# Kernel optimization log

Hardware: AMD Instinct MI355X
Metric: run time of the kernel (lower is better)

The kernel has to match this reference:

```python
import jax, jax.numpy as jnp
import numpy as np

N_LAYERS = 8
D_MODEL = 64
D_STATE = 32
D_CONV = 4
D_INNER = 128          # expand * d_model
HEADDIM = 64
NHEADS = D_INNER // HEADDIM      # 2
CONV_DIM = D_INNER + 2 * D_STATE # 192 (x, B, C)
D_IN_PROJ = 2 * D_INNER + 2 * D_STATE + NHEADS  # 322
EPS = 1e-5


def setup_inputs() -> dict:
    key = jax.random.key(0)
    ks = jax.random.split(key, 8)
    x = jax.random.normal(ks[0], (16, 4096, D_MODEL), dtype=jnp.float32)
    Win = jax.random.normal(ks[1], (N_LAYERS, D_MODEL, D_IN_PROJ), dtype=jnp.float32) * 0.05
    conv_w = jax.random.normal(ks[2], (N_LAYERS, CONV_DIM, D_CONV), dtype=jnp.float32) * 0.2
    conv_b = jnp.zeros((N_LAYERS, CONV_DIM), dtype=jnp.float32)
    dt_bias = jax.random.uniform(ks[3], (N_LAYERS, NHEADS), minval=-4.0, maxval=-1.0)
    A_log = jnp.log(jax.random.uniform(ks[4], (N_LAYERS, NHEADS), minval=1.0, maxval=16.0))
    Dp = jnp.ones((N_LAYERS, NHEADS), dtype=jnp.float32)
    norm_w = jnp.ones((N_LAYERS, D_INNER), dtype=jnp.float32)
    Wout = jax.random.normal(ks[5], (N_LAYERS, D_INNER, D_MODEL), dtype=jnp.float32) * 0.05
    return {"x": x, "Win": Win, "conv_w": conv_w, "conv_b": conv_b,
            "dt_bias": dt_bias, "A_log": A_log, "Dp": Dp,
            "norm_w": norm_w, "Wout": Wout}


def _mamba2_layer(u, Win, conv_w, conv_b, dt_bias, A_log, Dp, norm_w, Wout):
    b, l, _ = u.shape
    zxbcdt = u @ Win                                   # (b,l,322)
    z = zxbcdt[..., :D_INNER]                          # gate (b,l,128)
    xBC = zxbcdt[..., D_INNER:D_INNER + CONV_DIM]      # (b,l,192)
    dt = jax.nn.softplus(zxbcdt[..., D_INNER + CONV_DIM:] + dt_bias)  # (b,l,H)

    # causal depthwise conv over time, then SiLU
    xc = jnp.pad(xBC.transpose(0, 2, 1), ((0, 0), (0, 0), (D_CONV - 1, 0)))
    xc = jax.lax.conv_general_dilated(
        xc, conv_w[:, None, :], (1,), 'VALID',
        feature_group_count=CONV_DIM,
        dimension_numbers=('NCH', 'OIH', 'NCH'))
    xBC = jax.nn.silu((xc + conv_b[None, :, None]).transpose(0, 2, 1))  # (b,l,192)

    xs = xBC[..., :D_INNER].reshape(b, l, NHEADS, HEADDIM)   # (b,l,h,p)
    B = xBC[..., D_INNER:D_INNER + D_STATE]                  # (b,l,n)
    C = xBC[..., D_INNER + D_STATE:]                         # (b,l,n)

    A = -jnp.exp(A_log)                                      # (h,) negative
    dA = jnp.exp(dt * A)                                     # (b,l,h)

    # sequential selective scan over time; state (b,h,p,n)
    def step(hst, inp):
        dA_t, dt_t, x_t, B_t, C_t = inp
        hst = hst * dA_t[:, :, None, None] + \
              (dt_t[:, :, None] * x_t)[..., None] * B_t[:, None, None, :]
        y_t = jnp.einsum('bhpn,bn->bhp', hst, C_t)
        return hst, y_t

    h0 = jnp.zeros((b, NHEADS, HEADDIM, D_STATE), dtype=u.dtype)
    seq = (jnp.moveaxis(dA, 1, 0), jnp.moveaxis(dt, 1, 0),
           jnp.moveaxis(xs, 1, 0), jnp.moveaxis(B, 1, 0), jnp.moveaxis(C, 1, 0))
    _, ys = jax.lax.scan(step, h0, seq)                      # (l,b,h,p)
    y = jnp.moveaxis(ys, 0, 1) + Dp[None, None, :, None] * xs  # (b,l,h,p)
    y = y.reshape(b, l, D_INNER)

    # gated RMSNorm (norm_before_gate=False): normalize after gating
    y = y * jax.nn.silu(z)
    y = y * jax.lax.rsqrt(jnp.mean(y * y, axis=-1, keepdims=True) + EPS) * norm_w
    return y @ Wout                                          # (b,l,d_model)


def reference(x, Win, conv_w, conv_b, dt_bias, A_log, Dp, norm_w, Wout):
    h = x
    for i in range(N_LAYERS - 1):
        h = _mamba2_layer(h, Win[i], conv_w[i], conv_b[i], dt_bias[i],
                          A_log[i], Dp[i], norm_w[i], Wout[i])
    h = jax.lax.stop_gradient(h)  # layers[:-1] run under torch.no_grad()
    i = N_LAYERS - 1
    return _mamba2_layer(h, Win[i], conv_w[i], conv_b[i], dt_bias[i],
                         A_log[i], Dp[i], norm_w[i], Wout[i])
```

## Files before the change

kernel.cpp:

```cpp
#include <hip/hip_runtime.h>
#include <math.h>

#define BATCH   16
#define SEQ     4096
#define DMODEL  64
#define DINNER  128
#define DSTATE  32
#define NHEADS  2
#define HEADDIM 64
#define CONVDIM 192
#define PROJ    322
#define QC      64
#define NCHUNK  (SEQ/QC)
#define BL      (BATCH*SEQ)
#define NPAD    336

typedef __attribute__((ext_vector_type(8))) short short8;
typedef __attribute__((ext_vector_type(4))) float f32x4;
typedef __attribute__((ext_vector_type(4))) unsigned short ushort4v;

__device__ inline unsigned short f2b(float f){
  union { float f; unsigned u; } v; v.f = f;
  unsigned r = v.u + 0x7FFF + ((v.u >> 16) & 1);
  return (unsigned short)(r >> 16);
}
__device__ inline float b2f(unsigned short s){
  union { unsigned u; float f; } v; v.u = ((unsigned)s) << 16; return v.f;
}
__device__ inline void split2(float x, unsigned short& h, unsigned short& l){
  unsigned short hh = f2b(x);
  h = hh;
  l = f2b(x - b2f(hh));
}

__device__ float g_z   [(size_t)BL*DINNER];
__device__ float g_y   [(size_t)BL*DINNER];
__device__ unsigned short g_C[(size_t)BL*DSTATE];
__device__ float g_dt  [BATCH*NHEADS*SEQ];
__device__ float g_cum [BATCH*NHEADS*SEQ];
__device__ float g_ctot[BATCH*NHEADS*NCHUNK];
__device__ float g_S   [BATCH*NHEADS*NCHUNK*DSTATE*HEADDIM];
__device__ float g_H   [BATCH*NHEADS*NCHUNK*DSTATE*HEADDIM];
__device__ float g_ping0[(size_t)BL*DMODEL];
__device__ float g_ping1[(size_t)BL*DMODEL];
__device__ unsigned short g_WinTh [8*NPAD*DMODEL];
__device__ unsigned short g_WinTl [8*NPAD*DMODEL];
__device__ unsigned short g_WoutTh[8*DMODEL*DINNER];
__device__ unsigned short g_WoutTl[8*DMODEL*DINNER];

__global__ __launch_bounds__(256) void k_prep(const float* __restrict__ Win,
                                              const float* __restrict__ Wout,
                                              const float* __restrict__ normw) {
  const int idx = blockIdx.x*256 + threadIdx.x;
  const int NW = 8*NPAD*DMODEL;
  if (idx < NW) {
    int layer = idx / (NPAD*DMODEL);
    int rem   = idx - layer*(NPAD*DMODEL);
    int n = rem >> 6, k = rem & 63;
    float v = (n < PROJ) ? Win[(size_t)layer*DMODEL*PROJ + k*PROJ + n] : 0.f;
    split2(v, g_WinTh[idx], g_WinTl[idx]);
  } else {
    int i2 = idx - NW;
    if (i2 < 8*DMODEL*DINNER) {
      int layer = i2 / (DMODEL*DINNER);
      int rem   = i2 - layer*(DMODEL*DINNER);
      int n = rem >> 7, k = rem & 127;
      float v = Wout[(size_t)layer*DINNER*DMODEL + k*DMODEL + n] * normw[layer*DINNER + k];
      split2(v, g_WoutTh[i2], g_WoutTl[i2]);
    }
  }
}

__global__ __launch_bounds__(256,3) void k_fusedAB(const float* __restrict__ xext, int sel,
                                                   const unsigned short* __restrict__ WinTh,
                                                   const unsigned short* __restrict__ WinTl,
                                                   const float* __restrict__ Win,
                                                   const float* __restrict__ dt_bias,
                                                   const float* __restrict__ A_log,
                                                   const float* __restrict__ conv_w,
                                                   const float* __restrict__ conv_b,
                                                   const float* __restrict__ Dp) {
  __shared__ struct {
    unsigned short Xt[64][72];
    unsigned short Bt[32][72];
    float Hl[2][5][3][68];
    union {
      struct { unsigned short Bsh[64][40]; unsigned short Csh[64][40]; } bc;
      unsigned short Gsh[64][72];
    } u;
    float cumS[64]; float dtS[64]; float ewlS[64];
  } S_;

  const float* __restrict__ X = (sel==0) ? xext : (sel==1 ? g_ping0 : g_ping1);
  const int bx = blockIdx.x; const int b = bx>>7, h = (bx>>6)&1, ch = bx&63;
  const int tid = threadIdx.x;
  const int w = tid>>6, l = tid&63, lane15 = l&15, quad = l>>4;
  const size_t row0 = (size_t)b*SEQ + (size_t)ch*QC;
  const int cbase = (b*NHEADS+h)*SEQ + ch*QC;
  const float dph = Dp[h];

  const float* xrow = &X[(row0 + 16*w + lane15)*DMODEL + quad*8];
  float4 f0 = *(const float4*)(xrow);
  float4 f1 = *(const float4*)(xrow + 4);
  float4 f2 = *(const float4*)(xrow + 32);
  float4 f3 = *(const float4*)(xrow + 36);
  short8 a0h, a0l, a1h, a1l;
  {
    float v0[8] = {f0.x,f0.y,f0.z,f0.w,f1.x,f1.y,f1.z,f1.w};
    float v1[8] = {f2.x,f2.y,f2.z,f2.w,f3.x,f3.y,f3.z,f3.w};
    unsigned short hh, ll;
#pragma unroll
    for (int j=0;j<8;j++){ split2(v0[j], hh, ll); a0h[j]=(short)hh; a0l[j]=(short)ll; }
#pragma unroll
    for (int j=0;j<8;j++){ split2(v1[j], hh, ll); a1h[j]=(short)hh; a1l[j]=(short)ll; }
  }

  auto MFMA6 = [&](short8 A0h, short8 A1h, short8 A0l, short8 A1l, int t)->f32x4 {
    const unsigned short* bph = &WinTh[(16*t + lane15)*64 + quad*8];
    const unsigned short* bpl = &WinTl[(16*t + lane15)*64 + quad*8];
    short8 b0h = *(const short8*)bph;
    short8 b1h = *(const short8*)(bph + 32);
    short8 b0l = *(const short8*)bpl;
    short8 b1l = *(const short8*)(bpl + 32);
    f32x4 acc = {0.f,0.f,0.f,0.f};
    acc = __builtin_amdgcn_mfma_f32_16x16x32_bf16(A0h, b0h, acc, 0, 0, 0);
    acc = __builtin_amdgcn_mfma_f32_16x16x32_bf16(A1h, b1h, acc, 0, 0, 0);
    acc = __builtin_amdgcn_mfma_f32_16x16x32_bf16(A0l, b0h, acc, 0, 0, 0);
    acc = __builtin_amdgcn_mfma_f32_16x16x32_bf16(A1l, b1h, acc, 0, 0, 0);
    acc = __builtin_amdgcn_mfma_f32_16x16x32_bf16(A0h, b0l, acc, 0, 0, 0);
    acc = __builtin_amdgcn_mfma_f32_16x16x32_bf16(A1h, b1l, acc, 0, 0, 0);
    return acc;
  };

  if (w == 0) {
    const int t = l;
    float acc = 0.f;
    const float* xr = &X[(row0+t)*DMODEL];
#pragma unroll
    for (int k=0;k<64;k++) acc = fmaf(xr[k], Win[k*PROJ + (DINNER+CONVDIM) + h], acc);
    float xv = acc + dt_bias[h];
    float dtv = (xv > 20.f) ? xv : log1pf(expf(xv));
    float A = -expf(A_log[h]);
    float cum = dtv * A;
#pragma unroll
    for (int off=1; off<64; off<<=1){
      float v = __shfl_up(cum, off);
      if (t >= off) cum += v;
    }
    g_dt [cbase+t] = dtv;
    g_cum[cbase+t] = cum;
    if (t == 63) g_ctot[(b*NHEADS+h)*NCHUNK + ch] = cum;
    float cl = __shfl(cum, 63);
    S_.cumS[t] = cum;
    S_.dtS[t]  = dtv;
    S_.ewlS[t] = expf(cl - cum) * dtv;
  }

  if (ch != 0){
    const float* xh = &X[(row0 - 16 + lane15)*DMODEL + quad*8];
    float4 g0 = *(const float4*)(xh);
    float4 g1 = *(const float4*)(xh + 4);
    float4 g2 = *(const float4*)(xh + 32);
    float4 g3 = *(const float4*)(xh + 36);
    short8 e0h, e0l, e1h, e1l;
    {
      float v0[8] = {g0.x,g0.y,g0.z,g0.w,g1.x,g1.y,g1.z,g1.w};
      float v1[8] = {g2.x,g2.y,g2.z,g2.w,g3.x,g3.y,g3.z,g3.w};
      unsigned short hh, ll;
#pragma unroll
      for (int j=0;j<8;j++){ split2(v0[j], hh, ll); e0h[j]=(short)hh; e0l[j]=(short)ll; }
#pragma unroll
      for (int j=0;j<8;j++){ split2(v1[j], hh, ll); e1h[j]=(short)hh; e1l[j]=(short)ll; }
    }
    f32x4 hA = MFMA6(e0h, e1h, e0l, e1l, 8+4*h+w);
    f32x4 hB = MFMA6(e0h, e1h, e0l, e1l, 16+w);
    if (quad == 3){
#pragma unroll
      for (int r=1;r<4;r++){
        S_.Hl[0][4][r-1][w*16+lane15] = hA[r];
        S_.Hl[1][4][r-1][w*16+lane15] = hB[r];
      }
    }
  } else if (tid < 192) {
    int j = tid>>6, n = tid&63;
    S_.Hl[0][4][j][n] = 0.f;
    S_.Hl[1][4][j][n] = 0.f;
  }

  f32x4 pa[4];
#pragma unroll
  for (int tt=0; tt<4; tt++) pa[tt] = MFMA6(a0h, a1h, a0l, a1l, 8+4*h+tt);
  if (quad == 3){
#pragma unroll
    for (int tt=0; tt<4; tt++)
#pragma unroll
      for (int r=1;r<4;r++)
        S_.Hl[0][w][r-1][tt*16+lane15] = pa[tt][r];
  }
  __syncthreads();

  const int t0 = 16*w + quad*4;
  float sv[4][4];
#pragma unroll
  for (int tt=0; tt<4; tt++){
    const int n = tt*16 + lane15;
    const int gch = h*64 + n;
    const float w0 = conv_w[gch*4+0], w1 = conv_w[gch*4+1], w2 = conv_w[gch*4+2], w3 = conv_w[gch*4+3];
    const float bb = conv_b[gch];
    float o0 = pa[tt][0], o1 = pa[tt][1], o2 = pa[tt][2], o3 = pa[tt][3];
    float p1 = __shfl_up(o3, 16), p2 = __shfl_up(o2, 16), p3 = __shfl_up(o1, 16);
    if (quad == 0){
      const int slot = (w==0) ? 4 : (w-1);
      p1 = S_.Hl[0][slot][2][n];
      p2 = S_.Hl[0][slot][1][n];
      p3 = S_.Hl[0][slot][0][n];
    }
    float c0 = fmaf(w0,p3, fmaf(w1,p2, fmaf(w2,p1, fmaf(w3,o0, bb))));
    float c1 = fmaf(w0,p2, fmaf(w1,p1, fmaf(w2,o0, fmaf(w3,o1, bb))));
    float c2 = fmaf(w0,p1, fmaf(w1,o0, fmaf(w2,o1, fmaf(w3,o2, bb))));
    float c3 = fmaf(w0,o0, fmaf(w1,o1, fmaf(w2,o2, fmaf(w3,o3, bb))));
    sv[tt][0] = c0 / (1.f + expf(-c0));
    sv[tt][1] = c1 / (1.f + expf(-c1));
    sv[tt][2] = c2 / (1.f + expf(-c2));
    sv[tt][3] = c3 / (1.f + expf(-c3));
    ushort4v xq = { f2b(sv[tt][0]), f2b(sv[tt][1]), f2b(sv[tt][2]), f2b(sv[tt][3]) };
    *(ushort4v*)&S_.Xt[n][t0] = xq;
  }

  f32x4 pb[4];
#pragma unroll
  for (int tt=0; tt<4; tt++) pb[tt] = MFMA6(a0h, a1h, a0l, a1l, 16+tt);
  if (quad == 3){
#pragma unroll
    for (int tt=0; tt<4; tt++)
#pragma unroll
      for (int r=1;r<4;r++)
        S_.Hl[1][w][r-1][tt*16+lane15] = pb[tt][r];
  }
  __syncthreads();

  {
    float ew0 = S_.ewlS[t0+0], ew1 = S_.ewlS[t0+1], ew2 = S_.ewlS[t0+2], ew3 = S_.ewlS[t0+3];
#pragma unroll
    for (int tt=0; tt<4; tt++){
      const int nf = tt*16 + lane15;
      const int gch = 128 + nf;
      const float w0 = conv_w[gch*4+0], w1 = conv_w[gch*4+1], w2 = conv_w[gch*4+2], w3 = conv_w[gch*4+3];
      const float bb = conv_b[gch];
      float o0 = pb[tt][0], o1 = pb[tt][1], o2 = pb[tt][2], o3 = pb[tt][3];
      float p1 = __shfl_up(o3, 16), p2 = __shfl_up(o2, 16), p3 = __shfl_up(o1, 16);
      if (quad == 0){
        const int slot = (w==0) ? 4 : (w-1);
        p1 = S_.Hl[1][slot][2][nf];
        p2 = S_.Hl[1][slot][1][nf];
        p3 = S_.Hl[1][slot][0][nf];
      }
      float c0 = fmaf(w0,p3, fmaf(w1,p2, fmaf(w2,p1, fmaf(w3,o0, bb))));
      float c1 = fmaf(w0,p2, fmaf(w1,p1, fmaf(w2,o0, fmaf(w3,o1, bb))));
      float c2 = fmaf(w0,p1, fmaf(w1,o0, fmaf(w2,o1, fmaf(w3,o2, bb))));
      float c3 = fmaf(w0,o0, fmaf(w1,o1, fmaf(w2,o2, fmaf(w3,o3, bb))));
      float s0 = c0 / (1.f + expf(-c0));
      float s1 = c1 / (1.f + expf(-c1));
      float s2 = c2 / (1.f + expf(-c2));
      float s3 = c3 / (1.f + expf(-c3));
      if (tt < 2){
        const int n = nf;
        S_.u.bc.Bsh[t0+0][n] = f2b(s0);
        S_.u.bc.Bsh[t0+1][n] = f2b(s1);
        S_.u.bc.Bsh[t0+2][n] = f2b(s2);
        S_.u.bc.Bsh[t0+3][n] = f2b(s3);
        ushort4v bq = { f2b(s0*ew0), f2b(s1*ew1), f2b(s2*ew2), f2b(s3*ew3) };
        *(ushort4v*)&S_.Bt[n][t0] = bq;
      } else {
        const int n = nf - 32;
        S_.u.bc.Csh[t0+0][n] = f2b(s0);
        S_.u.bc.Csh[t0+1][n] = f2b(s1);
        S_.u.bc.Csh[t0+2][n] = f2b(s2);
        S_.u.bc.Csh[t0+3][n] = f2b(s3);
        if (h == 0){
          g_C[(row0+t0+0)*DSTATE + n] = f2b(s0);
          g_C[(row0+t0+1)*DSTATE + n] = f2b(s1);
          g_C[(row0+t0+2)*DSTATE + n] = f2b(s2);
          g_C[(row0+t0+3)*DSTATE + n] = f2b(s3);
        }
      }
    }
  }
  __syncthreads();

  short8 afr = *(const short8*)&S_.u.bc.Csh[16*w + lane15][quad*8];
  f32x4 gacc[4];
#pragma unroll
  for (int tn=0;tn<4;tn++){
    short8 bfr = *(const short8*)&S_.u.bc.Bsh[16*tn + lane15][quad*8];
    f32x4 z = {0.f,0.f,0.f,0.f};
    gacc[tn] = __builtin_amdgcn_mfma_f32_16x16x32_bf16(afr, bfr, z, 0, 0, 0);
  }
  __syncthreads();
#pragma unroll
  for (int tn=0;tn<4;tn++){
    int s = 16*tn + lane15;
    float cs = S_.cumS[s], ds = S_.dtS[s];
#pragma unroll
    for (int r=0;r<4;r++){
      int t = 16*w + quad*4 + r;
      float gv = 0.f;
      if (s <= t) gv = expf(S_.cumS[t]-cs) * ds * gacc[tn][r];
      S_.u.Gsh[t][s] = f2b(gv);
    }
  }
  __syncthreads();
#pragma unroll
  for (int tn=0;tn<4;tn++){
    f32x4 acc = {0.f,0.f,0.f,0.f};
#pragma unroll
    for (int ks=0;ks<2;ks++){
      short8 a  = *(const short8*)&S_.u.Gsh[16*w  + lane15][quad*8 + 32*ks];
      short8 bf = *(const short8*)&S_.Xt  [16*tn + lane15][quad*8 + 32*ks];
      acc = __builtin_amdgcn_mfma_f32_16x16x32_bf16(a, bf, acc, 0, 0, 0);
    }
    int p = 16*tn + lane15;
#pragma unroll
    for (int r=0;r<4;r++){
      int t = 16*w + quad*4 + r;
      g_y[(row0+t)*DINNER + h*HEADDIM + p] = acc[r] + dph * sv[tn][r];
    }
  }
  const size_t sb = (size_t)((b*NHEADS+h)*NCHUNK + ch) * (DSTATE*HEADDIM);
  const int tm2 = w & 1, tnb = (w>>1)*2;
#pragma unroll
  for (int tt=0;tt<2;tt++){
    int tn2 = tnb + tt;
    f32x4 acc = {0.f,0.f,0.f,0.f};
#pragma unroll
    for (int ks=0;ks<2;ks++){
      short8 a  = *(const short8*)&S_.Bt[16*tm2 + lane15][quad*8 + 32*ks];
      short8 bf = *(const short8*)&S_.Xt[16*tn2 + lane15][quad*8 + 32*ks];
      acc = __builtin_amdgcn_mfma_f32_16x16x32_bf16(a, bf, acc, 0, 0, 0);
    }
    int p = 16*tn2 + lane15;
#pragma unroll
    for (int r=0;r<4;r++){
      int n = 16*tm2 + quad*4 + r;
      g_S[sb + n*HEADDIM + p] = acc[r];
    }
  }

  f32x4 az[4];
#pragma unroll
  for (int tt=0; tt<4; tt++) az[tt] = MFMA6(a0h, a1h, a0l, a1l, 4*h+tt);
  __syncthreads();
  {
    float (*stg)[68] = (float(*)[68])((float*)&S_ + (size_t)w*16*68);
#pragma unroll
    for (int tt=0; tt<4; tt++)
#pragma unroll
      for (int r=0;r<4;r++)
        stg[quad*4+r][tt*16+lane15] = az[tt][r];
#pragma unroll
    for (int it=0; it<4; it++){
      int e = it*64 + l;
      int lr = e>>4, c4 = (e&15)<<2;
      float4 v = *(const float4*)&stg[lr][c4];
      *(float4*)&g_z[(row0 + 16*w + lr)*DINNER + h*64 + c4] = v;
    }
  }
}

__global__ __launch_bounds__(256) void k_chunkScan() {
  __shared__ float dAc[NCHUNK];
  const int idx = blockIdx.x*256 + threadIdx.x;
  const int np = idx & 2047;
  const int bh = idx >> 11;
  if (threadIdx.x < NCHUNK) dAc[threadIdx.x] = expf(g_ctot[bh*NCHUNK + threadIdx.x]);
  __syncthreads();
  float h = 0.f;
  const size_t base = (size_t)bh*NCHUNK*2048 + np;
#pragma unroll 1
  for (int k0=0; k0<NCHUNK; k0+=8){
    float s[8];
#pragma unroll
    for (int j=0;j<8;j++) s[j] = g_S[base + (size_t)(k0+j)*2048];
    float hs[8];
#pragma unroll
    for (int j=0;j<8;j++){
      hs[j] = h;
      h = h*dAc[k0+j] + s[j];
    }
#pragma unroll
    for (int j=0;j<8;j++) g_H[base + (size_t)(k0+j)*2048] = hs[j];
  }
}

__global__ __launch_bounds__(256,3) void k_fusedC(const unsigned short* __restrict__ WoutTh,
                                                  const unsigned short* __restrict__ WoutTl,
                                                  float* __restrict__ dout, int dsel) {
  __shared__ float Cl[QC][DSTATE+1];
  __shared__ float ec[NHEADS][QC];
  __shared__ unsigned short yAh[64][136];
  __shared__ unsigned short yAl[64][136];
  float* __restrict__ out = (dsel==0) ? g_ping0 : (dsel==1 ? g_ping1 : dout);
  const int bx = blockIdx.x; const int b = bx>>6, ch = bx&63;
  const int tid = threadIdx.x;
  const size_t row0 = (size_t)b*SEQ + (size_t)ch*QC;
  const int w = tid>>6, l = tid&63, lane15 = l&15, quad = l>>4;
#pragma unroll
  for (int j=0;j<8;j++){ int e=tid+j*256; int s=e>>5, n=e&31;
    Cl[s][n] = b2f(g_C[(row0+s)*DSTATE + n]); }
  if (tid < 128){ int h_=tid>>6, s=tid&63;
    ec[h_][s] = expf(g_cum[(b*NHEADS+h_)*SEQ + ch*QC + s]); }
  float hr[64];
  {
    const float* H0 = &g_H[(size_t)((b*NHEADS+0)*NCHUNK + ch)*2048];
    const float* H1 = &g_H[(size_t)((b*NHEADS+1)*NCHUNK + ch)*2048];
#pragma unroll
    for (int n=0;n<32;n++){ hr[n] = H0[n*64 + l]; hr[32+n] = H1[n*64 + l]; }
  }
  __syncthreads();
#pragma unroll 1
  for (int i=0;i<16;i++){
    const int r = 16*w + i;
    const size_t row = row0 + r;
    float d0 = 0.f, d1 = 0.f;
#pragma unroll
    for (int n=0;n<32;n++){
      float c = Cl[r][n];
      d0 = fmaf(c, hr[n],    d0);
      d1 = fmaf(c, hr[32+n], d1);
    }
    float yv0 = g_y[row*DINNER + l]      + ec[0][r]*d0;
    float yv1 = g_y[row*DINNER + l + 64] + ec[1][r]*d1;
    float z0 = g_z[row*DINNER + l];
    float z1 = g_z[row*DINNER + l + 64];
    yv0 *= z0 / (1.f + expf(-z0));
    yv1 *= z1 / (1.f + expf(-z1));
    float ss = yv0*yv0 + yv1*yv1;
#pragma unroll
    for (int off=32; off>=1; off>>=1) ss += __shfl_xor(ss, off);
    float sc = rsqrtf(ss*(1.f/128.f) + 1e-5f);
    split2(yv0*sc, yAh[r][l],    yAl[r][l]);
    split2(yv1*sc, yAh[r][l+64], yAl[r][l+64]);
  }
  __syncthreads();
  short8 afh[4], afl[4];
#pragma unroll
  for (int ks=0;ks<4;ks++){
    afh[ks] = *(const short8*)&yAh[16*w + lane15][quad*8 + 32*ks];
    afl[ks] = *(const short8*)&yAl[16*w + lane15][quad*8 + 32*ks];
  }
  __syncthreads();
  float (*stgF)[68] = (float(*)[68])((float*)&yAh[0][0] + (size_t)w*16*68);
#pragma unroll
  for (int tc=0;tc<4;tc++){
    f32x4 acc = {0.f,0.f,0.f,0.f};
#pragma unroll
    for (int ks=0;ks<4;ks++){
      const unsigned short* bph = &WoutTh[(16*tc + lane15)*DINNER + quad*8 + 32*ks];
      const unsigned short* bpl = &WoutTl[(16*tc + lane15)*DINNER + quad*8 + 32*ks];
      short8 bh  = *(const short8*)bph;
      short8 blo = *(const short8*)bpl;
      acc = __builtin_amdgcn_mfma_f32_16x16x32_bf16(afh[ks], bh,  acc, 0, 0, 0);
      acc = __builtin_amdgcn_mfma_f32_16x16x32_bf16(afl[ks], bh,  acc, 0, 0, 0);
      acc = __builtin_amdgcn_mfma_f32_16x16x32_bf16(afh[ks], blo, acc, 0, 0, 0);
    }
#pragma unroll
    for (int r=0;r<4;r++)
      stgF[quad*4+r][tc*16+lane15] = acc[r];
  }
#pragma unroll
  for (int it=0; it<4; it++){
    int e = it*64 + l;
    int lr = e>>4, c4 = (e&15)<<2;
    float4 v = *(const float4*)&stgF[lr][c4];
    *(float4*)&out[(row0 + 16*w + lr)*DMODEL + c4] = v;
  }
}

extern "C" void kernel_launch(void* const* d_in, const int* in_sizes, int n_in,
                              void* d_out, int out_size, void* d_ws, size_t ws_size,
                              hipStream_t stream) {
  (void)in_sizes; (void)n_in; (void)d_ws; (void)ws_size; (void)out_size;
  const float* x       = (const float*)d_in[0];
  const float* Win     = (const float*)d_in[1];
  const float* conv_w  = (const float*)d_in[2];
  const float* conv_b  = (const float*)d_in[3];
  const float* dt_bias = (const float*)d_in[4];
  const float* A_log   = (const float*)d_in[5];
  const float* Dp      = (const float*)d_in[6];
  const float* norm_w  = (const float*)d_in[7];
  const float* Wout    = (const float*)d_in[8];

  k_prep<<<(8*(NPAD*DMODEL + DMODEL*DINNER) + 255)/256, 256, 0, stream>>>(Win, Wout, norm_w);

  unsigned short *winTh, *winTl, *woutTh, *woutTl;
  hipGetSymbolAddress((void**)&winTh,  HIP_SYMBOL(g_WinTh));
  hipGetSymbolAddress((void**)&winTl,  HIP_SYMBOL(g_WinTl));
  hipGetSymbolAddress((void**)&woutTh, HIP_SYMBOL(g_WoutTh));
  hipGetSymbolAddress((void**)&woutTl, HIP_SYMBOL(g_WoutTl));

  for (int layer = 0; layer < 8; ++layer) {
    const int insel = (layer==0) ? 0 : ((((layer-1)&1)==0) ? 1 : 2);
    const int dsel  = (layer==7) ? 2 : ((layer&1)==0 ? 0 : 1);

    k_fusedAB<<<BATCH*NHEADS*NCHUNK, 256, 0, stream>>>(x, insel,
                                        winTh + (size_t)layer*NPAD*DMODEL,
                                        winTl + (size_t)layer*NPAD*DMODEL,
                                        Win + (size_t)layer*DMODEL*PROJ,
                                        dt_bias + layer*NHEADS, A_log + layer*NHEADS,
                                        conv_w + (size_t)layer*CONVDIM*4,
                                        conv_b + (size_t)layer*CONVDIM,
                                        Dp + layer*NHEADS);
    k_chunkScan<<<(BATCH*NHEADS*DSTATE*HEADDIM)/256, 256, 0, stream>>>();
    k_fusedC<<<BATCH*NCHUNK, 256, 0, stream>>>(woutTh + (size_t)layer*DMODEL*DINNER,
                                               woutTl + (size_t)layer*DMODEL*DINNER,
                                               (float*)d_out, dsel);
  }
}
```

Measured before the change: 1.179 ms.

## Replace shared-memory halo and scan staging with wave shuffles, drop barriers

Every wave now computes the dt/cumsum scan redundantly instead of wave 0 writing it to shared memory. Each wave also computes its own 16-row halo projection and fetches the conv history via cross-lane shuffles, which removes the Hl halo buffer and several __syncthreads. The z projection is written straight to global memory without the staged coalesced store, and the unused g_dt write is dropped. Shared memory shrinks and launch bounds rise to 4 blocks per CU. The cost is extra redundant MFMA and scan work per wave, higher register pressure, and uncoalesced scalar stores for g_z.

```diff
diff --git a/kernel.cpp b/kernel.cpp
--- a/kernel.cpp
+++ b/kernel.cpp
@@ -36,7 +36,6 @@
 __device__ float g_z   [(size_t)BL*DINNER];
 __device__ float g_y   [(size_t)BL*DINNER];
 __device__ unsigned short g_C[(size_t)BL*DSTATE];
-__device__ float g_dt  [BATCH*NHEADS*SEQ];
 __device__ float g_cum [BATCH*NHEADS*SEQ];
 __device__ float g_ctot[BATCH*NHEADS*NCHUNK];
 __device__ float g_S   [BATCH*NHEADS*NCHUNK*DSTATE*HEADDIM];
@@ -71,7 +70,7 @@
   }
 }
 
-__global__ __launch_bounds__(256,3) void k_fusedAB(const float* __restrict__ xext, int sel,
+__global__ __launch_bounds__(256,4) void k_fusedAB(const float* __restrict__ xext, int sel,
                                                    const unsigned short* __restrict__ WinTh,
                                                    const unsigned short* __restrict__ WinTl,
                                                    const float* __restrict__ Win,
@@ -81,14 +80,11 @@
                                                    const float* __restrict__ conv_b,
                                                    const float* __restrict__ Dp) {
   __shared__ struct {
-    unsigned short Xt[64][72];
-    unsigned short Bt[32][72];
-    float Hl[2][5][3][68];
-    union {
-      struct { unsigned short Bsh[64][40]; unsigned short Csh[64][40]; } bc;
-      unsigned short Gsh[64][72];
-    } u;
-    float cumS[64]; float dtS[64]; float ewlS[64];
+    unsigned short Xt [64][72];
+    unsigned short Bt [32][72];
+    unsigned short Bsh[64][40];
+    unsigned short Csh[64][40];
+    unsigned short Gsh[64][72];
   } S_;
 
   const float* __restrict__ X = (sel==0) ? xext : (sel==1 ? g_ping0 : g_ping1);
@@ -113,6 +109,30 @@
     for (int j=0;j<8;j++){ split2(v0[j], hh, ll); a0h[j]=(short)hh; a0l[j]=(short)ll; }
 #pragma unroll
     for (int j=0;j<8;j++){ split2(v1[j], hh, ll); a1h[j]=(short)hh; a1l[j]=(short)ll; }
+  }
+
+  float cum, dtv, ewl;
+  {
+    const int t = l;
+    float acc = 0.f;
+    const float* xr = &X[(row0+t)*DMODEL];
+#pragma unroll
+    for (int k=0;k<64;k++) acc = fmaf(xr[k], Win[k*PROJ + (DINNER+CONVDIM) + h], acc);
+    float xv = acc + dt_bias[h];
+    dtv = (xv > 20.f) ? xv : log1pf(expf(xv));
+    float A = -expf(A_log[h]);
+    cum = dtv * A;
+#pragma unroll
+    for (int off=1; off<64; off<<=1){
+      float v = __shfl_up(cum, off);
+      if (t >= off) cum += v;
+    }
+    if (w == 0){
+      g_cum[cbase+t] = cum;
+      if (t == 63) g_ctot[(b*NHEADS+h)*NCHUNK + ch] = cum;
+    }
+    float cl = __shfl(cum, 63);
+    ewl = expf(cl - cum) * dtv;
   }
 
   auto MFMA6 = [&](short8 A0h, short8 A1h, short8 A0l, short8 A1l, int t)->f32x4 {
@@ -132,32 +152,10 @@
     return acc;
   };
 
-  if (w == 0) {
-    const int t = l;
-    float acc = 0.f;
-    const float* xr = &X[(row0+t)*DMODEL];
-#pragma unroll
-    for (int k=0;k<64;k++) acc = fmaf(xr[k], Win[k*PROJ + (DINNER+CONVDIM) + h], acc);
-    float xv = acc + dt_bias[h];
-    float dtv = (xv > 20.f) ? xv : log1pf(expf(xv));
-    float A = -expf(A_log[h]);
-    float cum = dtv * A;
-#pragma unroll
-    for (int off=1; off<64; off<<=1){
-      float v = __shfl_up(cum, off);
-      if (t >= off) cum += v;
-    }
-    g_dt [cbase+t] = dtv;
-    g_cum[cbase+t] = cum;
-    if (t == 63) g_ctot[(b*NHEADS+h)*NCHUNK + ch] = cum;
-    float cl = __shfl(cum, 63);
-    S_.cumS[t] = cum;
-    S_.dtS[t]  = dtv;
-    S_.ewlS[t] = expf(cl - cum) * dtv;
-  }
-
-  if (ch != 0){
-    const float* xh = &X[(row0 - 16 + lane15)*DMODEL + quad*8];
+  const bool hvalid = (ch > 0) || (w > 0);
+  f32x4 hA[4], hB[4];
+  if (hvalid){
+    const float* xh = &X[(row0 + 16*w - 16 + lane15)*DMODEL + quad*8];
     float4 g0 = *(const float4*)(xh);
     float4 g1 = *(const float4*)(xh + 4);
     float4 g2 = *(const float4*)(xh + 32);
@@ -172,34 +170,35 @@
 #pragma unroll
       for (int j=0;j<8;j++){ split2(v1[j], hh, ll); e1h[j]=(short)hh; e1l[j]=(short)ll; }
     }
-    f32x4 hA = MFMA6(e0h, e1h, e0l, e1l, 8+4*h+w);
-    f32x4 hB = MFMA6(e0h, e1h, e0l, e1l, 16+w);
-    if (quad == 3){
-#pragma unroll
-      for (int r=1;r<4;r++){
-        S_.Hl[0][4][r-1][w*16+lane15] = hA[r];
-        S_.Hl[1][4][r-1][w*16+lane15] = hB[r];
-      }
-    }
-  } else if (tid < 192) {
-    int j = tid>>6, n = tid&63;
-    S_.Hl[0][4][j][n] = 0.f;
-    S_.Hl[1][4][j][n] = 0.f;
+#pragma unroll
+    for (int tt=0; tt<4; tt++) hA[tt] = MFMA6(e0h, e1h, e0l, e1l, 8+4*h+tt);
+#pragma unroll
+    for (int tt=0; tt<4; tt++) hB[tt] = MFMA6(e0h, e1h, e0l, e1l, 16+tt);
+  } else {
+    f32x4 zz = {0.f,0.f,0.f,0.f};
+#pragma unroll
+    for (int tt=0; tt<4; tt++){ hA[tt] = zz; hB[tt] = zz; }
+  }
+
+  {
+#pragma unroll
+    for (int tt=0; tt<4; tt++){
+      f32x4 az = MFMA6(a0h, a1h, a0l, a1l, 4*h+tt);
+#pragma unroll
+      for (int r=0;r<4;r++)
+        g_z[(row0 + 16*w + quad*4 + r)*DINNER + h*64 + tt*16 + lane15] = az[r];
+    }
   }
 
   f32x4 pa[4];
 #pragma unroll
   for (int tt=0; tt<4; tt++) pa[tt] = MFMA6(a0h, a1h, a0l, a1l, 8+4*h+tt);
-  if (quad == 3){
-#pragma unroll
-    for (int tt=0; tt<4; tt++)
-#pragma unroll
-      for (int r=1;r<4;r++)
-        S_.Hl[0][w][r-1][tt*16+lane15] = pa[tt][r];
-  }
-  __syncthreads();
+  f32x4 pb[4];
+#pragma unroll
+  for (int tt=0; tt<4; tt++) pb[tt] = MFMA6(a0h, a1h, a0l, a1l, 16+tt);
 
   const int t0 = 16*w + quad*4;
+
   float sv[4][4];
 #pragma unroll
   for (int tt=0; tt<4; tt++){
@@ -209,12 +208,10 @@
     const float bb = conv_b[gch];
     float o0 = pa[tt][0], o1 = pa[tt][1], o2 = pa[tt][2], o3 = pa[tt][3];
     float p1 = __shfl_up(o3, 16), p2 = __shfl_up(o2, 16), p3 = __shfl_up(o1, 16);
-    if (quad == 0){
-      const int slot = (w==0) ? 4 : (w-1);
-      p1 = S_.Hl[0][slot][2][n];
-      p2 = S_.Hl[0][slot][1][n];
-      p3 = S_.Hl[0][slot][0][n];
-    }
+    float q1 = __shfl(hA[tt][3], 48+lane15);
+    float q2 = __shfl(hA[tt][2], 48+lane15);
+    float q3 = __shfl(hA[tt][1], 48+lane15);
+    if (quad == 0){ p1 = q1; p2 = q2; p3 = q3; }
     float c0 = fmaf(w0,p3, fmaf(w1,p2, fmaf(w2,p1, fmaf(w3,o0, bb))));
     float c1 = fmaf(w0,p2, fmaf(w1,p1, fmaf(w2,o0, fmaf(w3,o1, bb))));
     float c2 = fmaf(w0,p1, fmaf(w1,o0, fmaf(w2,o1, fmaf(w3,o2, bb))));
@@ -227,20 +224,9 @@
     *(ushort4v*)&S_.Xt[n][t0] = xq;
   }
 
-  f32x4 pb[4];
-#pragma unroll
-  for (int tt=0; tt<4; tt++) pb[tt] = MFMA6(a0h, a1h, a0l, a1l, 16+tt);
-  if (quad == 3){
-#pragma unroll
-    for (int tt=0; tt<4; tt++)
-#pragma unroll
-      for (int r=1;r<4;r++)
-        S_.Hl[1][w][r-1][tt*16+lane15] = pb[tt][r];
-  }
-  __syncthreads();
-
   {
-    float ew0 = S_.ewlS[t0+0], ew1 = S_.ewlS[t0+1], ew2 = S_.ewlS[t0+2], ew3 = S_.ewlS[t0+3];
+    float ew0 = __shfl(ewl, t0+0), ew1 = __shfl(ewl, t0+1);
+    float ew2 = __shfl(ewl, t0+2), ew3 = __shfl(ewl, t0+3);
 #pragma unroll
     for (int tt=0; tt<4; tt++){
       const int nf = tt*16 + lane15;
@@ -249,12 +235,10 @@
       const float bb = conv_b[gch];
       float o0 = pb[tt][0], o1 = pb[tt][1], o2 = pb[tt][2], o3 = pb[tt][3];
       float p1 = __shfl_up(o3, 16), p2 = __shfl_up(o2, 16), p3 = __shfl_up(o1, 16);
-      if (quad == 0){
-        const int slot = (w==0) ? 4 : (w-1);
-        p1 = S_.Hl[1][slot][2][nf];
-        p2 = S_.Hl[1][slot][1][nf];
-        p3 = S_.Hl[1][slot][0][nf];
-      }
+      float q1 = __shfl(hB[tt][3], 48+lane15);
+      float q2 = __shfl(hB[tt][2], 48+lane15);
+      float q3 = __shfl(hB[tt][1], 48+lane15);
+      if (quad == 0){ p1 = q1; p2 = q2; p3 = q3; }
       float c0 = fmaf(w0,p3, fmaf(w1,p2, fmaf(w2,p1, fmaf(w3,o0, bb))));
       float c1 = fmaf(w0,p2, fmaf(w1,p1, fmaf(w2,o0, fmaf(w3,o1, bb))));
       float c2 = fmaf(w0,p1, fmaf(w1,o0, fmaf(w2,o1, fmaf(w3,o2, bb))));
@@ -265,18 +249,18 @@
       float s3 = c3 / (1.f + expf(-c3));
       if (tt < 2){
         const int n = nf;
-        S_.u.bc.Bsh[t0+0][n] = f2b(s0);
-        S_.u.bc.Bsh[t0+1][n] = f2b(s1);
-        S_.u.bc.Bsh[t0+2][n] = f2b(s2);
-        S_.u.bc.Bsh[t0+3][n] = f2b(s3);
+        S_.Bsh[t0+0][n] = f2b(s0);
+        S_.Bsh[t0+1][n] = f2b(s1);
+        S_.Bsh[t0+2][n] = f2b(s2);
+        S_.Bsh[t0+3][n] = f2b(s3);
         ushort4v bq = { f2b(s0*ew0), f2b(s1*ew1), f2b(s2*ew2), f2b(s3*ew3) };
         *(ushort4v*)&S_.Bt[n][t0] = bq;
       } else {
         const int n = nf - 32;
-        S_.u.bc.Csh[t0+0][n] = f2b(s0);
-        S_.u.bc.Csh[t0+1][n] = f2b(s1);
-        S_.u.bc.Csh[t0+2][n] = f2b(s2);
-        S_.u.bc.Csh[t0+3][n] = f2b(s3);
+        S_.Csh[t0+0][n] = f2b(s0);
+        S_.Csh[t0+1][n] = f2b(s1);
+        S_.Csh[t0+2][n] = f2b(s2);
+        S_.Csh[t0+3][n] = f2b(s3);
         if (h == 0){
           g_C[(row0+t0+0)*DSTATE + n] = f2b(s0);
           g_C[(row0+t0+1)*DSTATE + n] = f2b(s1);
@@ -288,25 +272,25 @@
   }
   __syncthreads();
 
-  short8 afr = *(const short8*)&S_.u.bc.Csh[16*w + lane15][quad*8];
+  short8 afr = *(const short8*)&S_.Csh[16*w + lane15][quad*8];
   f32x4 gacc[4];
 #pragma unroll
   for (int tn=0;tn<4;tn++){
-    short8 bfr = *(const short8*)&S_.u.bc.Bsh[16*tn + lane15][quad*8];
+    short8 bfr = *(const short8*)&S_.Bsh[16*tn + lane15][quad*8];
     f32x4 z = {0.f,0.f,0.f,0.f};
     gacc[tn] = __builtin_amdgcn_mfma_f32_16x16x32_bf16(afr, bfr, z, 0, 0, 0);
   }
-  __syncthreads();
 #pragma unroll
   for (int tn=0;tn<4;tn++){
     int s = 16*tn + lane15;
-    float cs = S_.cumS[s], ds = S_.dtS[s];
+    float cs = __shfl(cum, s), ds = __shfl(dtv, s);
 #pragma unroll
     for (int r=0;r<4;r++){
       int t = 16*w + quad*4 + r;
+      float ct = __shfl(cum, t);
       float gv = 0.f;
-      if (s <= t) gv = expf(S_.cumS[t]-cs) * ds * gacc[tn][r];
-      S_.u.Gsh[t][s] = f2b(gv);
+      if (s <= t) gv = expf(ct-cs) * ds * gacc[tn][r];
+      S_.Gsh[t][s] = f2b(gv);
     }
   }
   __syncthreads();
@@ -315,8 +299,8 @@
     f32x4 acc = {0.f,0.f,0.f,0.f};
 #pragma unroll
     for (int ks=0;ks<2;ks++){
-      short8 a  = *(const short8*)&S_.u.Gsh[16*w  + lane15][quad*8 + 32*ks];
-      short8 bf = *(const short8*)&S_.Xt  [16*tn + lane15][quad*8 + 32*ks];
+      short8 a  = *(const short8*)&S_.Gsh[16*w  + lane15][quad*8 + 32*ks];
+      short8 bf = *(const short8*)&S_.Xt [16*tn + lane15][quad*8 + 32*ks];
       acc = __builtin_amdgcn_mfma_f32_16x16x32_bf16(a, bf, acc, 0, 0, 0);
     }
     int p = 16*tn + lane15;
@@ -343,26 +327,6 @@
     for (int r=0;r<4;r++){
       int n = 16*tm2 + quad*4 + r;
       g_S[sb + n*HEADDIM + p] = acc[r];
-    }
-  }
-
-  f32x4 az[4];
-#pragma unroll
-  for (int tt=0; tt<4; tt++) az[tt] = MFMA6(a0h, a1h, a0l, a1l, 4*h+tt);
-  __syncthreads();
-  {
-    float (*stg)[68] = (float(*)[68])((float*)&S_ + (size_t)w*16*68);
-#pragma unroll
-    for (int tt=0; tt<4; tt++)
-#pragma unroll
-      for (int r=0;r<4;r++)
-        stg[quad*4+r][tt*16+lane15] = az[tt][r];
-#pragma unroll
-    for (int it=0; it<4; it++){
-      int e = it*64 + l;
-      int lr = e>>4, c4 = (e&15)<<2;
-      float4 v = *(const float4*)&stg[lr][c4];
-      *(float4*)&g_z[(row0 + 16*w + lr)*DINNER + h*64 + c4] = v;
     }
   }
 }
```

Measured after the change: 1.410 ms. 19.6% more time.

## Spread dt projection across all waves and restructure fused chunk kernel schedule

Applied to the files above, without the earlier changes.

The dt projection was computed serially by wave 0 with a 64-step dot product. It is now computed by every wave from the already-loaded x fragments, using partial dot products and cross-lane shuffle reductions. Each wave redundantly computes the cumulative-sum scan, so cum, dt and the decay weights come from lane shuffles instead of shared memory. The z output is written straight from MFMA registers instead of being staged through shared memory, the pb MFMAs move ahead of the first barrier so one __syncthreads disappears, the unused g_dt buffer is removed, and launch bounds rise to 4 blocks per CU. In exchange the z stores are less coalesced, the scan work is duplicated across four waves, and register pressure may spill under the tighter occupancy bound.

```diff
diff --git a/kernel.cpp b/kernel.cpp
--- a/kernel.cpp
+++ b/kernel.cpp
@@ -36,7 +36,6 @@
 __device__ float g_z   [(size_t)BL*DINNER];
 __device__ float g_y   [(size_t)BL*DINNER];
 __device__ unsigned short g_C[(size_t)BL*DSTATE];
-__device__ float g_dt  [BATCH*NHEADS*SEQ];
 __device__ float g_cum [BATCH*NHEADS*SEQ];
 __device__ float g_ctot[BATCH*NHEADS*NCHUNK];
 __device__ float g_S   [BATCH*NHEADS*NCHUNK*DSTATE*HEADDIM];
@@ -71,7 +70,7 @@
   }
 }
 
-__global__ __launch_bounds__(256,3) void k_fusedAB(const float* __restrict__ xext, int sel,
+__global__ __launch_bounds__(256,4) void k_fusedAB(const float* __restrict__ xext, int sel,
                                                    const unsigned short* __restrict__ WinTh,
                                                    const unsigned short* __restrict__ WinTl,
                                                    const float* __restrict__ Win,
@@ -81,14 +80,14 @@
                                                    const float* __restrict__ conv_b,
                                                    const float* __restrict__ Dp) {
   __shared__ struct {
-    unsigned short Xt[64][72];
-    unsigned short Bt[32][72];
+    unsigned short Xt [64][72];
+    unsigned short Bt [32][72];
     float Hl[2][5][3][68];
     union {
       struct { unsigned short Bsh[64][40]; unsigned short Csh[64][40]; } bc;
       unsigned short Gsh[64][72];
     } u;
-    float cumS[64]; float dtS[64]; float ewlS[64];
+    float dtraw[64];
   } S_;
 
   const float* __restrict__ X = (sel==0) ? xext : (sel==1 ? g_ping0 : g_ping1);
@@ -105,14 +104,26 @@
   float4 f2 = *(const float4*)(xrow + 32);
   float4 f3 = *(const float4*)(xrow + 36);
   short8 a0h, a0l, a1h, a1l;
+  float v0[8] = {f0.x,f0.y,f0.z,f0.w,f1.x,f1.y,f1.z,f1.w};
+  float v1[8] = {f2.x,f2.y,f2.z,f2.w,f3.x,f3.y,f3.z,f3.w};
   {
-    float v0[8] = {f0.x,f0.y,f0.z,f0.w,f1.x,f1.y,f1.z,f1.w};
-    float v1[8] = {f2.x,f2.y,f2.z,f2.w,f3.x,f3.y,f3.z,f3.w};
     unsigned short hh, ll;
 #pragma unroll
     for (int j=0;j<8;j++){ split2(v0[j], hh, ll); a0h[j]=(short)hh; a0l[j]=(short)ll; }
 #pragma unroll
     for (int j=0;j<8;j++){ split2(v1[j], hh, ll); a1h[j]=(short)hh; a1l[j]=(short)ll; }
+  }
+
+  {
+    const float* wd = &Win[DINNER + CONVDIM + h];
+    float p = 0.f;
+#pragma unroll
+    for (int j=0;j<8;j++) p = fmaf(v0[j], wd[(quad*8+j)*PROJ], p);
+#pragma unroll
+    for (int j=0;j<8;j++) p = fmaf(v1[j], wd[(32+quad*8+j)*PROJ], p);
+    p += __shfl_xor(p, 16);
+    p += __shfl_xor(p, 32);
+    if (quad == 0) S_.dtraw[16*w + lane15] = p;
   }
 
   auto MFMA6 = [&](short8 A0h, short8 A1h, short8 A0l, short8 A1l, int t)->f32x4 {
@@ -132,30 +143,6 @@
     return acc;
   };
 
-  if (w == 0) {
-    const int t = l;
-    float acc = 0.f;
-    const float* xr = &X[(row0+t)*DMODEL];
-#pragma unroll
-    for (int k=0;k<64;k++) acc = fmaf(xr[k], Win[k*PROJ + (DINNER+CONVDIM) + h], acc);
-    float xv = acc + dt_bias[h];
-    float dtv = (xv > 20.f) ? xv : log1pf(expf(xv));
-    float A = -expf(A_log[h]);
-    float cum = dtv * A;
-#pragma unroll
-    for (int off=1; off<64; off<<=1){
-      float v = __shfl_up(cum, off);
-      if (t >= off) cum += v;
-    }
-    g_dt [cbase+t] = dtv;
-    g_cum[cbase+t] = cum;
-    if (t == 63) g_ctot[(b*NHEADS+h)*NCHUNK + ch] = cum;
-    float cl = __shfl(cum, 63);
-    S_.cumS[t] = cum;
-    S_.dtS[t]  = dtv;
-    S_.ewlS[t] = expf(cl - cum) * dtv;
-  }
-
   if (ch != 0){
     const float* xh = &X[(row0 - 16 + lane15)*DMODEL + quad*8];
     float4 g0 = *(const float4*)(xh);
@@ -164,13 +151,13 @@
     float4 g3 = *(const float4*)(xh + 36);
     short8 e0h, e0l, e1h, e1l;
     {
-      float v0[8] = {g0.x,g0.y,g0.z,g0.w,g1.x,g1.y,g1.z,g1.w};
-      float v1[8] = {g2.x,g2.y,g2.z,g2.w,g3.x,g3.y,g3.z,g3.w};
+      float u0[8] = {g0.x,g0.y,g0.z,g0.w,g1.x,g1.y,g1.z,g1.w};
+      float u1[8] = {g2.x,g2.y,g2.z,g2.w,g3.x,g3.y,g3.z,g3.w};
       unsigned short hh, ll;
 #pragma unroll
-      for (int j=0;j<8;j++){ split2(v0[j], hh, ll); e0h[j]=(short)hh; e0l[j]=(short)ll; }
-#pragma unroll
-      for (int j=0;j<8;j++){ split2(v1[j], hh, ll); e1h[j]=(short)hh; e1l[j]=(short)ll; }
+      for (int j=0;j<8;j++){ split2(u0[j], hh, ll); e0h[j]=(short)hh; e0l[j]=(short)ll; }
+#pragma unroll
+      for (int j=0;j<8;j++){ split2(u1[j], hh, ll); e1h[j]=(short)hh; e1l[j]=(short)ll; }
     }
     f32x4 hA = MFMA6(e0h, e1h, e0l, e1l, 8+4*h+w);
     f32x4 hB = MFMA6(e0h, e1h, e0l, e1l, 16+w);
@@ -187,6 +174,16 @@
     S_.Hl[1][4][j][n] = 0.f;
   }
 
+  {
+#pragma unroll
+    for (int tt=0; tt<4; tt++){
+      f32x4 az = MFMA6(a0h, a1h, a0l, a1l, 4*h+tt);
+#pragma unroll
+      for (int r=0;r<4;r++)
+        g_z[(row0 + 16*w + quad*4 + r)*DINNER + h*64 + tt*16 + lane15] = az[r];
+    }
+  }
+
   f32x4 pa[4];
 #pragma unroll
   for (int tt=0; tt<4; tt++) pa[tt] = MFMA6(a0h, a1h, a0l, a1l, 8+4*h+tt);
@@ -197,9 +194,40 @@
       for (int r=1;r<4;r++)
         S_.Hl[0][w][r-1][tt*16+lane15] = pa[tt][r];
   }
-  __syncthreads();
+  f32x4 pb[4];
+#pragma unroll
+  for (int tt=0; tt<4; tt++) pb[tt] = MFMA6(a0h, a1h, a0l, a1l, 16+tt);
+  if (quad == 3){
+#pragma unroll
+    for (int tt=0; tt<4; tt++)
+#pragma unroll
+      for (int r=1;r<4;r++)
+        S_.Hl[1][w][r-1][tt*16+lane15] = pb[tt][r];
+  }
+  __syncthreads();
+
+  float cum, dtv, ewl;
+  {
+    float dr = S_.dtraw[l];
+    float xv = dr + dt_bias[h];
+    dtv = (xv > 20.f) ? xv : log1pf(expf(xv));
+    float A = -expf(A_log[h]);
+    cum = dtv * A;
+#pragma unroll
+    for (int off=1; off<64; off<<=1){
+      float v = __shfl_up(cum, off);
+      if (l >= off) cum += v;
+    }
+    if (w == 0){
+      g_cum[cbase+l] = cum;
+      if (l == 63) g_ctot[(b*NHEADS+h)*NCHUNK + ch] = cum;
+    }
+    float cl = __shfl(cum, 63);
+    ewl = expf(cl - cum) * dtv;
+  }
 
   const int t0 = 16*w + quad*4;
+
   float sv[4][4];
 #pragma unroll
   for (int tt=0; tt<4; tt++){
@@ -227,20 +255,9 @@
     *(ushort4v*)&S_.Xt[n][t0] = xq;
   }
 
-  f32x4 pb[4];
-#pragma unroll
-  for (int tt=0; tt<4; tt++) pb[tt] = MFMA6(a0h, a1h, a0l, a1l, 16+tt);
-  if (quad == 3){
-#pragma unroll
-    for (int tt=0; tt<4; tt++)
-#pragma unroll
-      for (int r=1;r<4;r++)
-        S_.Hl[1][w][r-1][tt*16+lane15] = pb[tt][r];
-  }
-  __syncthreads();
-
   {
-    float ew0 = S_.ewlS[t0+0], ew1 = S_.ewlS[t0+1], ew2 = S_.ewlS[t0+2], ew3 = S_.ewlS[t0+3];
+    float ew0 = __shfl(ewl, t0+0), ew1 = __shfl(ewl, t0+1);
+    float ew2 = __shfl(ewl, t0+2), ew3 = __shfl(ewl, t0+3);
 #pragma unroll
     for (int tt=0; tt<4; tt++){
       const int nf = tt*16 + lane15;
@@ -300,12 +317,13 @@
 #pragma unroll
   for (int tn=0;tn<4;tn++){
     int s = 16*tn + lane15;
-    float cs = S_.cumS[s], ds = S_.dtS[s];
+    float cs = __shfl(cum, s), ds = __shfl(dtv, s);
 #pragma unroll
     for (int r=0;r<4;r++){
       int t = 16*w + quad*4 + r;
+      float ct = __shfl(cum, t);
       float gv = 0.f;
-      if (s <= t) gv = expf(S_.cumS[t]-cs) * ds * gacc[tn][r];
+      if (s <= t) gv = expf(ct-cs) * ds * gacc[tn][r];
       S_.u.Gsh[t][s] = f2b(gv);
     }
   }
@@ -343,26 +361,6 @@
     for (int r=0;r<4;r++){
       int n = 16*tm2 + quad*4 + r;
       g_S[sb + n*HEADDIM + p] = acc[r];
-    }
-  }
-
-  f32x4 az[4];
-#pragma unroll
-  for (int tt=0; tt<4; tt++) az[tt] = MFMA6(a0h, a1h, a0l, a1l, 4*h+tt);
-  __syncthreads();
-  {
-    float (*stg)[68] = (float(*)[68])((float*)&S_ + (size_t)w*16*68);
-#pragma unroll
-    for (int tt=0; tt<4; tt++)
-#pragma unroll
-      for (int r=0;r<4;r++)
-        stg[quad*4+r][tt*16+lane15] = az[tt][r];
-#pragma unroll
-    for (int it=0; it<4; it++){
-      int e = it*64 + l;
-      int lr = e>>4, c4 = (e&15)<<2;
-      float4 v = *(const float4*)&stg[lr][c4];
-      *(float4*)&g_z[(row0 + 16*w + lr)*DINNER + h*64 + c4] = v;
     }
   }
 }
```

Result: no change. 1.161 ms (-1.5%).
